# Optimization experiments

Measured on AMD Instinct MI355X. Metric: run time of the kernel, lower is better.

The kernel has to match this reference:

```python
import jax, jax.numpy as jnp
import numpy as np

TEMP_LEN, TARGET_LEN = 16, 22
NT, NA = TEMP_LEN ** 2, TARGET_LEN ** 2  # 256, 484
N = NT + NA  # 740
DIM, HEADS = 512, 8
HD = DIM // HEADS
SCALE = HD ** -0.5
BATCH = 16


def _bias_index(L):
    # Swin-style relative position index for an LxL grid -> [L^2, L^2] ints
    coords = np.stack(np.meshgrid(np.arange(L), np.arange(L), indexing='ij')).reshape(2, -1)
    rel = (coords[:, :, None] - coords[:, None, :]).transpose(1, 2, 0).copy()
    rel[..., 0] += L - 1
    rel[..., 1] += L - 1
    rel[..., 0] *= 2 * L - 1
    return jnp.asarray(rel.sum(-1))


TEMP_IDX = _bias_index(TEMP_LEN)
TARGET_IDX = _bias_index(TARGET_LEN)


def _conv_bn(x, w, g, b, m, v):
    # depthwise 3x3 conv (groups=DIM), then BatchNorm in inference form
    y = jax.lax.conv_general_dilated(x, w, (1, 1), 'SAME', feature_group_count=DIM,
                                     dimension_numbers=('NCHW', 'OIHW', 'NCHW'))
    inv = g * jax.lax.rsqrt(v + 1e-5)
    return y * inv[None, :, None, None] + (b - m * inv)[None, :, None, None]


def _forward(x, wcq, wck, wcv,
             bnq_g, bnq_b, bnq_m, bnq_v,
             bnk_g, bnk_b, bnk_m, bnk_v,
             bnv_g, bnv_b, bnv_m, bnv_v,
             wq, wk, wv, wproj, bproj,
             rpb_target, rpb_temp, t2a_table, a2t_table, t2a_line, a2t_line):
    B = x.shape[0]
    temp = jnp.transpose(x[:, :NT], (0, 2, 1)).reshape(B, DIM, TEMP_LEN, TEMP_LEN)
    target = jnp.transpose(x[:, NT:], (0, 2, 1)).reshape(B, DIM, TARGET_LEN, TARGET_LEN)

    def proj_tokens(w, g, b, m, v):
        ytm = _conv_bn(temp, w, g, b, m, v).reshape(B, DIM, NT).transpose(0, 2, 1)
        yta = _conv_bn(target, w, g, b, m, v).reshape(B, DIM, NA).transpose(0, 2, 1)
        return jnp.concatenate([ytm, yta], axis=1)  # [B, N, DIM]

    q = proj_tokens(wcq, bnq_g, bnq_b, bnq_m, bnq_v)
    k = proj_tokens(wck, bnk_g, bnk_b, bnk_m, bnk_v)
    v = proj_tokens(wcv, bnv_g, bnv_b, bnv_m, bnv_v)

    # linear (no bias), split heads -> [B, H, N, HD]
    def heads(y, w):
        return jnp.einsum('bnc,dc->bnd', y, w).reshape(B, N, HEADS, HD).transpose(0, 2, 1, 3)

    q, k, v = heads(q, wq), heads(k, wk), heads(v, wv)

    # relative position bias, assembled blockwise -> [H, N, N]
    temp_b = rpb_temp[TEMP_IDX.reshape(-1)].reshape(NT, NT, HEADS).transpose(2, 0, 1)
    target_b = rpb_target[TARGET_IDX.reshape(-1)].reshape(NA, NA, HEADS).transpose(2, 0, 1)
    top_right = t2a_table + a2t_line    # [H, NT, NA] (temp queries -> target keys)
    bottom_left = a2t_table + t2a_line  # [H, NA, NT] (target queries -> temp keys)
    bias = jnp.concatenate([
        jnp.concatenate([temp_b, top_right], axis=2),
        jnp.concatenate([bottom_left, target_b], axis=2)], axis=1)

    attn = jnp.einsum('bhnd,bhmd->bhnm', q, k) * SCALE + bias[None]
    attn = jax.nn.softmax(attn, axis=-1)
    out = jnp.einsum('bhnm,bhmd->bhnd', attn, v).transpose(0, 2, 1, 3).reshape(B, N, DIM)
    return jnp.einsum('bnc,dc->bnd', out, wproj) + bproj


def setup_inputs() -> dict:
    key = jax.random.key(0)
    ks = jax.random.split(key, 32)
    d = {}
    d['x'] = jax.random.normal(ks[0], (BATCH, N, DIM), jnp.float32)
    for i, nm in enumerate(['q', 'k', 'v']):
        d['wc' + nm] = jax.random.normal(ks[1 + i], (DIM, 1, 3, 3), jnp.float32) * 0.1
        d['bn%s_g' % nm] = jax.random.uniform(ks[4 + i], (DIM,), jnp.float32, 0.5, 1.5)
        d['bn%s_b' % nm] = jax.random.normal(ks[7 + i], (DIM,), jnp.float32) * 0.1
        d['bn%s_m' % nm] = jax.random.normal(ks[10 + i], (DIM,), jnp.float32) * 0.1
        d['bn%s_v' % nm] = jax.random.uniform(ks[13 + i], (DIM,), jnp.float32, 0.5, 1.5)
        d['w' + nm] = jax.random.normal(ks[16 + i], (DIM, DIM), jnp.float32) * (DIM ** -0.5)
    d['wproj'] = jax.random.normal(ks[19], (DIM, DIM), jnp.float32) * (DIM ** -0.5)
    d['bproj'] = jnp.zeros((DIM,), jnp.float32)
    std = 0.0002
    d['rpb_target'] = jax.random.normal(ks[20], ((2 * TARGET_LEN - 1) ** 2, HEADS), jnp.float32) * std
    d['rpb_temp'] = jax.random.normal(ks[21], ((2 * TEMP_LEN - 1) ** 2, HEADS), jnp.float32) * std
    d['t2a_table'] = jax.random.normal(ks[22], (HEADS, NT, 1), jnp.float32) * std
    d['a2t_table'] = jax.random.normal(ks[23], (HEADS, NA, 1), jnp.float32) * std
    d['t2a_line'] = jax.random.normal(ks[24], (HEADS, 1, NT), jnp.float32) * std
    d['a2t_line'] = jax.random.normal(ks[25], (HEADS, 1, NA), jnp.float32) * std
    return d


def reference(x, wcq, wck, wcv,
              bnq_g, bnq_b, bnq_m, bnq_v,
              bnk_g, bnk_b, bnk_m, bnk_v,
              bnv_g, bnv_b, bnv_m, bnv_v,
              wq, wk, wv, wproj, bproj,
              rpb_target, rpb_temp, t2a_table, a2t_table, t2a_line, a2t_line):
    return _forward(x, wcq, wck, wcv,
                    bnq_g, bnq_b, bnq_m, bnq_v,
                    bnk_g, bnk_b, bnk_m, bnk_v,
                    bnv_g, bnv_b, bnv_m, bnv_v,
                    wq, wk, wv, wproj, bproj,
                    rpb_target, rpb_temp, t2a_table, a2t_table, t2a_line, a2t_line)
```

## Files before the change

### kernel.cpp

```cpp
#include <hip/hip_runtime.h>
#include <hip/hip_bf16.h>
#include <cstdint>
#include <cstddef>

typedef __hip_bfloat16 bf16;
typedef float  f32x4 __attribute__((ext_vector_type(4)));
typedef short  s16x8 __attribute__((ext_vector_type(8)));
typedef short  s16x4 __attribute__((ext_vector_type(4)));

#define NB    16
#define NTOK  740
#define NTMP  256
#define NTGT  484
#define DIM   512
#define NHEAD 8
#define HD    64
#define MROWS (NB*NTOK)
#define WOFF  (DIM*DIM)
#define BSTRIDE 768
#define LOG2E 1.44269504f
#define SC2   (0.125f * LOG2E)

#define EXP2F(x) __builtin_amdgcn_exp2f(x)

static __device__ __forceinline__ short f2bs(float f) {
    bf16 h = __float2bfloat16(f);
    return *reinterpret_cast<short*>(&h);
}
static __device__ __forceinline__ float bs2f(short s) {
    union { unsigned int u; float f; } cv;
    cv.u = ((unsigned int)(unsigned short)s) << 16;
    return cv.f;
}

__global__ __launch_bounds__(256) void convert_w_kernel(
    const float* __restrict__ wq, const float* __restrict__ wk,
    const float* __restrict__ wv, const float* __restrict__ wp,
    bf16* __restrict__ out)
{
    const int t = blockIdx.x * 256 + threadIdx.x;
    const int which = t >> 18;
    const int idx   = t & (WOFF - 1);
    const float* src = (which == 0) ? wq : (which == 1) ? wk : (which == 2) ? wv : wp;
    out[t] = __float2bfloat16(src[idx]);
}

__global__ __launch_bounds__(256) void prep_kernel(
    const float* __restrict__ wcq, const float* __restrict__ wck, const float* __restrict__ wcv,
    const float* __restrict__ qg, const float* __restrict__ qb, const float* __restrict__ qm, const float* __restrict__ qv,
    const float* __restrict__ kg, const float* __restrict__ kb, const float* __restrict__ km, const float* __restrict__ kv,
    const float* __restrict__ vg, const float* __restrict__ vb, const float* __restrict__ vm, const float* __restrict__ vv,
    float* __restrict__ wT, float* __restrict__ ss)
{
    const int t = blockIdx.x * 256 + threadIdx.x;
    if (t < 3 * 9 * 512) {
        const int w = t / (9 * 512);
        const int r = t - w * 9 * 512;
        const int s = r >> 9, c = r & 511;
        const float* src = (w == 0) ? wcq : (w == 1) ? wck : wcv;
        wT[t] = src[c * 9 + s];
    } else if (t < 3 * 9 * 512 + 3 * 512) {
        const int u = t - 3 * 9 * 512;
        const int w = u >> 9, c = u & 511;
        const float* G = (w == 0) ? qg : (w == 1) ? kg : vg;
        const float* V = (w == 0) ? qv : (w == 1) ? kv : vv;
        const float* B = (w == 0) ? qb : (w == 1) ? kb : vb;
        const float* M = (w == 0) ? qm : (w == 1) ? km : vm;
        const float inv = G[c] * rsqrtf(V[c] + 1e-5f);
        ss[w * 1024 + c]       = inv;
        ss[w * 1024 + 512 + c] = B[c] - M[c] * inv;
    }
}

__global__ __launch_bounds__(256) void bias_prep_kernel(
    const float* __restrict__ rpb_temp, const float* __restrict__ rpb_target,
    const float* __restrict__ t2a_tab, const float* __restrict__ a2t_tab,
    const float* __restrict__ t2a_line, const float* __restrict__ a2t_line,
    bf16* __restrict__ biasp)
{
    const int t = blockIdx.x * 256 + threadIdx.x;
    if (t >= NHEAD * NTOK * (BSTRIDE / 4)) return;
    const int kg = t % (BSTRIDE / 4);
    const int hq = t / (BSTRIDE / 4);
    const int qq = hq % NTOK;
    const int h  = hq / NTOK;

    bool tq; int qi, qj; float tab;
    if (qq < NTMP) { tq = true;  qi = qq >> 4; qj = qq & 15; tab = t2a_tab[h * NTMP + qq]; }
    else { tq = false; int qa = qq - NTMP; qi = qa / 22; qj = qa - qi * 22; tab = a2t_tab[h * NTGT + qa]; }

    s16x4 o;
    #pragma unroll
    for (int r = 0; r < 4; ++r) {
        const int key = kg * 4 + r;
        float bias = 0.f;
        if (key < NTOK) {
            if (tq) {
                if (key < NTMP) {
                    const int ki = key >> 4, kj = key & 15;
                    bias = rpb_temp[((qi - ki + 15) * 31 + (qj - kj + 15)) * NHEAD + h];
                } else bias = tab + a2t_line[h * NTGT + key - NTMP];
            } else {
                if (key < NTMP) bias = tab + t2a_line[h * NTMP + key];
                else {
                    const int ka = key - NTMP;
                    const int ki = ka / 22, kj = ka - ki * 22;
                    bias = rpb_target[((qi - ki + 21) * 43 + (qj - kj + 21)) * NHEAD + h];
                }
            }
        }
        o[r] = f2bs(bias * LOG2E);
    }
    *reinterpret_cast<s16x4*>(biasp + ((size_t)h * NTOK + qq) * BSTRIDE + kg * 4) = o;
}

__global__ __launch_bounds__(256) void conv_bn_kernel(
    const float* __restrict__ x,
    const float* __restrict__ wT, const float* __restrict__ ss,
    bf16* __restrict__ qc, bf16* __restrict__ kc, bf16* __restrict__ vc)
{
    const int t   = blockIdx.x * 256 + threadIdx.x;
    const int c0  = (t & 127) * 4;
    const int idx = t >> 7;
    const int b   = idx / NTOK;
    const int n   = idx - b * NTOK;

    int li, lj, L, base;
    if (n < NTMP) { L = 16; li = n >> 4; lj = n & 15; base = 0; }
    else          { int a = n - NTMP; L = 22; li = a / 22; lj = a - li * 22; base = NTMP; }

    const float* xb = x + (size_t)b * NTOK * DIM + c0;

    float4 xs[9];
    #pragma unroll
    for (int di = -1; di <= 1; ++di)
        #pragma unroll
        for (int dj = -1; dj <= 1; ++dj) {
            int ii = li + di, jj = lj + dj;
            float4 xv = make_float4(0.f, 0.f, 0.f, 0.f);
            if ((unsigned)ii < (unsigned)L && (unsigned)jj < (unsigned)L)
                xv = *reinterpret_cast<const float4*>(xb + (size_t)(base + ii * L + jj) * DIM);
            xs[(di + 1) * 3 + (dj + 1)] = xv;
        }

#define DO_CONV(OUT, W)                                                        \
    if (OUT) {                                                                 \
        float4 acc = make_float4(0.f, 0.f, 0.f, 0.f);                          \
        _Pragma("unroll")                                                      \
        for (int s = 0; s < 9; ++s) {                                          \
            const float4 w4 = *reinterpret_cast<const float4*>(wT + (W) * 4608 + s * 512 + c0); \
            acc.x += xs[s].x * w4.x; acc.y += xs[s].y * w4.y;                  \
            acc.z += xs[s].z * w4.z; acc.w += xs[s].w * w4.w;                  \
        }                                                                      \
        const float4 iv = *reinterpret_cast<const float4*>(ss + (W) * 1024 + c0);        \
        const float4 sh = *reinterpret_cast<const float4*>(ss + (W) * 1024 + 512 + c0);  \
        ushort4 o;                                                             \
        o.x = (unsigned short)f2bs(acc.x * iv.x + sh.x);                       \
        o.y = (unsigned short)f2bs(acc.y * iv.y + sh.y);                       \
        o.z = (unsigned short)f2bs(acc.z * iv.z + sh.z);                       \
        o.w = (unsigned short)f2bs(acc.w * iv.w + sh.w);                       \
        *reinterpret_cast<ushort4*>(OUT + (size_t)idx * DIM + c0) = o;         \
    }
    DO_CONV(qc, 0)
    DO_CONV(kc, 1)
    DO_CONV(vc, 2)
#undef DO_CONV
}

__global__ __launch_bounds__(256) void gemm_bt(
    const bf16* __restrict__ Abase,
    const bf16* __restrict__ W0, const bf16* __restrict__ W1, const bf16* __restrict__ W2,
    bf16* __restrict__ Cbase, float* __restrict__ Cf, const float* __restrict__ bias)
{
    __shared__ bf16 lA[128 * 32];
    __shared__ bf16 lB[128 * 32];

    const int tid  = threadIdx.x;
    const int lane = tid & 63;
    const int wid  = tid >> 6;
    const int lq   = lane & 15, lg = lane >> 4;
    const int wr   = wid >> 1,  wc = wid & 1;
    const int z    = blockIdx.z;

    const bf16* A = Abase + (size_t)z * MROWS * DIM;
    const bf16* W = (z == 0) ? W0 : ((z == 1) ? W1 : W2);
    bf16*       C = Cbase ? (Cbase + (size_t)z * MROWS * DIM) : nullptr;

    const int bm = blockIdx.x, bn = blockIdx.y;

    const int srow = wid * 16 + (lane >> 2);
    const int scol = (lane & 3) * 8;
    const int rowA0 = min(bm * 128 + srow,      MROWS - 1);
    const int rowA1 = min(bm * 128 + 64 + srow, MROWS - 1);
    const int rowB0 = bn * 128 + srow;
    const int rowB1 = rowB0 + 64;

    f32x4 acc[4][4];
    #pragma unroll
    for (int m = 0; m < 4; ++m)
        #pragma unroll
        for (int n = 0; n < 4; ++n) acc[m][n] = (f32x4){0.f, 0.f, 0.f, 0.f};

    for (int ks = 0; ks < 16; ++ks) {
        const int k0 = ks * 32 + scol;
        __builtin_amdgcn_global_load_lds(
            (const __attribute__((address_space(1))) void*)(A + (size_t)rowA0 * DIM + k0),
            (__attribute__((address_space(3))) void*)(lA + wid * 512), 16, 0, 0);
        __builtin_amdgcn_global_load_lds(
            (const __attribute__((address_space(1))) void*)(A + (size_t)rowA1 * DIM + k0),
            (__attribute__((address_space(3))) void*)(lA + (wid + 4) * 512), 16, 0, 0);
        __builtin_amdgcn_global_load_lds(
            (const __attribute__((address_space(1))) void*)(W + (size_t)rowB0 * DIM + k0),
            (__attribute__((address_space(3))) void*)(lB + wid * 512), 16, 0, 0);
        __builtin_amdgcn_global_load_lds(
            (const __attribute__((address_space(1))) void*)(W + (size_t)rowB1 * DIM + k0),
            (__attribute__((address_space(3))) void*)(lB + (wid + 4) * 512), 16, 0, 0);
        __syncthreads();

        s16x8 af[4], bf_[4];
        #pragma unroll
        for (int m = 0; m < 4; ++m)
            af[m] = *reinterpret_cast<const s16x8*>(&lA[(wr * 64 + m * 16 + lq) * 32 + lg * 8]);
        #pragma unroll
        for (int n = 0; n < 4; ++n)
            bf_[n] = *reinterpret_cast<const s16x8*>(&lB[(wc * 64 + n * 16 + lq) * 32 + lg * 8]);

        #pragma unroll
        for (int m = 0; m < 4; ++m)
            #pragma unroll
            for (int n = 0; n < 4; ++n)
                acc[m][n] = __builtin_amdgcn_mfma_f32_16x16x32_bf16(af[m], bf_[n], acc[m][n], 0, 0, 0);
        __syncthreads();
    }

    #pragma unroll
    for (int m = 0; m < 4; ++m) {
        const int row = bm * 128 + wr * 64 + m * 16 + lg * 4;
        #pragma unroll
        for (int n = 0; n < 4; ++n) {
            const int col = bn * 128 + wc * 64 + n * 16 + lq;
            const float bv = bias ? bias[col] : 0.f;
            #pragma unroll
            for (int r = 0; r < 4; ++r) {
                const int rr = row + r;
                if (rr < MROWS) {
                    const float val = acc[m][n][r] + bv;
                    if (Cf) Cf[(size_t)rr * DIM + col] = val;
                    else    C [(size_t)rr * DIM + col] = __float2bfloat16(val);
                }
            }
        }
    }
}

__global__ __launch_bounds__(256) void attn_kernel(
    const bf16* __restrict__ q, const bf16* __restrict__ k, const bf16* __restrict__ v,
    const bf16* __restrict__ biasp,
    bf16* __restrict__ out)
{
    __shared__ char  lK[64 * 128];
    __shared__ short lVT[64 * 72];

    const int lane = threadIdx.x & 63;
    const int wid  = threadIdx.x >> 6;
    const int lq   = lane & 15, lg = lane >> 4;
    const int h    = blockIdx.y, b = blockIdx.z;

    const size_t bh = (size_t)b * NTOK * DIM + h * HD;
    const bf16* qp = q + bh;
    const bf16* kp = k + bh;
    const bf16* vp = v + bh;

    const int qrA = blockIdx.x * 128 + wid * 32 + lq;
    const int qrB = qrA + 16;
    const int qA  = min(qrA, NTOK - 1);
    const int qB  = min(qrB, NTOK - 1);

    const s16x8 qf0A = *reinterpret_cast<const s16x8*>(qp + (size_t)qA * DIM + lg * 8);
    const s16x8 qf1A = *reinterpret_cast<const s16x8*>(qp + (size_t)qA * DIM + 32 + lg * 8);
    const s16x8 qf0B = *reinterpret_cast<const s16x8*>(qp + (size_t)qB * DIM + lg * 8);
    const s16x8 qf1B = *reinterpret_cast<const s16x8*>(qp + (size_t)qB * DIM + 32 + lg * 8);

    const bf16* bpA = biasp + ((size_t)h * NTOK + qA) * BSTRIDE;
    const bf16* bpB = biasp + ((size_t)h * NTOK + qB) * BSTRIDE;

    float mA = -1e30f, lsA = 0.f, mB = -1e30f, lsB = 0.f;
    f32x4 oA[4], oB[4];
    #pragma unroll
    for (int d = 0; d < 4; ++d) { oA[d] = (f32x4){0,0,0,0}; oB[d] = (f32x4){0,0,0,0}; }

    const int swz     = (((lane & 7) ^ (lane >> 3)) << 4);
    const int krowoff = lane >> 3;

    for (int t = 0; t < 12; ++t) {
        const int kt0 = t * 64;
        __syncthreads();

        #pragma unroll
        for (int c0 = 0; c0 < 2; ++c0) {
            const int c    = wid + c0 * 4;
            const int krow = min(kt0 + c * 8 + krowoff, NTOK - 1);
            __builtin_amdgcn_global_load_lds(
                (const __attribute__((address_space(1))) void*)((const char*)(kp + (size_t)krow * DIM) + swz),
                (__attribute__((address_space(3))) void*)(lK + c * 1024), 16, 0, 0);
        }
        {
            const int vrow = min(kt0 + lane, NTOK - 1);
            const bf16* vsrc = vp + (size_t)vrow * DIM + wid * 16;
            const s16x8 v0 = *reinterpret_cast<const s16x8*>(vsrc);
            const s16x8 v1 = *reinterpret_cast<const s16x8*>(vsrc + 8);
            #pragma unroll
            for (int i = 0; i < 8; ++i) {
                lVT[(wid * 16 + i)     * 72 + lane] = v0[i];
                lVT[(wid * 16 + 8 + i) * 72 + lane] = v1[i];
            }
        }
        s16x4 bA[4], bB[4];
        #pragma unroll
        for (int s = 0; s < 4; ++s) {
            bA[s] = *reinterpret_cast<const s16x4*>(bpA + kt0 + s * 16 + lg * 4);
            bB[s] = *reinterpret_cast<const s16x4*>(bpB + kt0 + s * 16 + lg * 4);
        }
        __syncthreads();

        f32x4 stA[4], stB[4];
        #pragma unroll
        for (int s = 0; s < 4; ++s) {
            const int row = s * 16 + lq;
            const int cb0 = (lg * 16)      ^ ((row & 7) << 4);
            const int cb1 = (64 + lg * 16) ^ ((row & 7) << 4);
            const s16x8 kf0 = *reinterpret_cast<const s16x8*>(lK + row * 128 + cb0);
            const s16x8 kf1 = *reinterpret_cast<const s16x8*>(lK + row * 128 + cb1);
            f32x4 z0 = {0,0,0,0}, z1 = {0,0,0,0};
            z0 = __builtin_amdgcn_mfma_f32_16x16x32_bf16(kf0, qf0A, z0, 0, 0, 0);
            stA[s] = __builtin_amdgcn_mfma_f32_16x16x32_bf16(kf1, qf1A, z0, 0, 0, 0);
            z1 = __builtin_amdgcn_mfma_f32_16x16x32_bf16(kf0, qf0B, z1, 0, 0, 0);
            stB[s] = __builtin_amdgcn_mfma_f32_16x16x32_bf16(kf1, qf1B, z1, 0, 0, 0);
        }

        s16x4 pbA[4], pbB[4];

#define TILE_SOFTMAX(ST, BV, MR, LS, OO, PB)                                    \
        {                                                                       \
            float tmax = -1e30f;                                                \
            _Pragma("unroll")                                                   \
            for (int s = 0; s < 4; ++s) {                                       \
                _Pragma("unroll")                                               \
                for (int r = 0; r < 4; ++r) {                                   \
                    float sv = ST[s][r] * SC2 + bs2f(BV[s][r]);                 \
                    if (kt0 + s * 16 + lg * 4 + r >= NTOK) sv = -1e30f;         \
                    ST[s][r] = sv;                                              \
                    tmax = fmaxf(tmax, sv);                                     \
                }                                                               \
            }                                                                   \
            tmax = fmaxf(tmax, __shfl_xor(tmax, 16));                           \
            tmax = fmaxf(tmax, __shfl_xor(tmax, 32));                           \
            if (tmax > MR) {                                                    \
                const float al = EXP2F(MR - tmax);                              \
                LS *= al;                                                       \
                _Pragma("unroll")                                               \
                for (int d = 0; d < 4; ++d) {                                   \
                    OO[d][0] *= al; OO[d][1] *= al;                             \
                    OO[d][2] *= al; OO[d][3] *= al;                             \
                }                                                               \
                MR = tmax;                                                      \
            }                                                                   \
            float rs = 0.f;                                                     \
            _Pragma("unroll")                                                   \
            for (int s = 0; s < 4; ++s) {                                       \
                _Pragma("unroll")                                               \
                for (int r = 0; r < 4; ++r) {                                   \
                    const float p = EXP2F(ST[s][r] - MR);                       \
                    rs += p;                                                    \
                    PB[s][r] = f2bs(p);                                         \
                }                                                               \
            }                                                                   \
            rs += __shfl_xor(rs, 16);                                           \
            rs += __shfl_xor(rs, 32);                                           \
            LS += rs;                                                           \
        }
        TILE_SOFTMAX(stA, bA, mA, lsA, oA, pbA)
        TILE_SOFTMAX(stB, bB, mB, lsB, oB, pbB)
#undef TILE_SOFTMAX

        #pragma unroll
        for (int s = 0; s < 4; ++s) {
            #pragma unroll
            for (int db = 0; db < 4; ++db) {
                const s16x4 av = *reinterpret_cast<const s16x4*>(
                    lVT + (db * 16 + lq) * 72 + s * 16 + lg * 4);
                oA[db] = __builtin_amdgcn_mfma_f32_16x16x16bf16_1k(av, pbA[s], oA[db], 0, 0, 0);
                oB[db] = __builtin_amdgcn_mfma_f32_16x16x16bf16_1k(av, pbB[s], oB[db], 0, 0, 0);
            }
        }
    }

#define STORE_FRAG(QR, LS, OO)                                                  \
    if ((QR) < NTOK) {                                                          \
        const float inv = 1.f / (LS);                                           \
        bf16* op = out + ((size_t)b * NTOK + (QR)) * DIM + h * HD;              \
        _Pragma("unroll")                                                       \
        for (int db = 0; db < 4; ++db) {                                        \
            ushort4 sv;                                                         \
            sv.x = (unsigned short)f2bs(OO[db][0] * inv);                       \
            sv.y = (unsigned short)f2bs(OO[db][1] * inv);                       \
            sv.z = (unsigned short)f2bs(OO[db][2] * inv);                       \
            sv.w = (unsigned short)f2bs(OO[db][3] * inv);                       \
            *reinterpret_cast<ushort4*>(op + db * 16 + lg * 4) = sv;            \
        }                                                                       \
    }
    STORE_FRAG(qrA, lsA, oA)
    STORE_FRAG(qrB, lsB, oB)
#undef STORE_FRAG
}

extern "C" void kernel_launch(void* const* d_in, const int* in_sizes, int n_in,
                              void* d_out, int out_size, void* d_ws, size_t ws_size,
                              hipStream_t stream)
{
    const bool sig = (in_sizes[2] == 4608);
    const float *x, *wcq, *wck, *wcv, *wq, *wk, *wv, *wproj, *bproj;
    const float *bnqg, *bnqb, *bnqm, *bnqv, *bnkg, *bnkb, *bnkm, *bnkv, *bnvg, *bnvb, *bnvm, *bnvv;
#define P(i) ((const float*)d_in[i])
    x = P(0);
    if (!sig) {
        wcq = P(1);  bnqg = P(2);  bnqb = P(3);  bnqm = P(4);  bnqv = P(5);  wq = P(6);
        wck = P(7);  bnkg = P(8);  bnkb = P(9);  bnkm = P(10); bnkv = P(11); wk = P(12);
        wcv = P(13); bnvg = P(14); bnvb = P(15); bnvm = P(16); bnvv = P(17); wv = P(18);
    } else {
        wcq = P(1);  wck = P(2);  wcv = P(3);
        bnqg = P(4);  bnqb = P(5);  bnqm = P(6);  bnqv = P(7);
        bnkg = P(8);  bnkb = P(9);  bnkm = P(10); bnkv = P(11);
        bnvg = P(12); bnvb = P(13); bnvm = P(14); bnvv = P(15);
        wq = P(16); wk = P(17); wv = P(18);
    }
    wproj = P(19); bproj = P(20);
    const float* rpbt = P(21);
    const float* rpbm = P(22);
    const float* t2at = P(23);
    const float* a2tt = P(24);
    const float* t2al = P(25);
    const float* a2tl = P(26);
#undef P

    const size_t BUF    = (size_t)MROWS * DIM;
    const size_t WELEMS = (size_t)4 * WOFF;
    const size_t PREPF  = 17408;
    const size_t BIASE  = (size_t)NHEAD * NTOK * BSTRIDE;

    bf16*  wsW   = (bf16*)d_ws;
    float* wsF   = (float*)(wsW + WELEMS);
    float* wT    = wsF;
    float* ssb   = wsF + 3 * 9 * 512;
    bf16*  biasP = (bf16*)(wsF + PREPF);
    bf16*  bufs  = biasP + BIASE;

    convert_w_kernel<<<dim3(WELEMS / 256), 256, 0, stream>>>(wq, wk, wv, wproj, wsW);
    prep_kernel<<<dim3(60), 256, 0, stream>>>(
        wcq, wck, wcv,
        bnqg, bnqb, bnqm, bnqv, bnkg, bnkb, bnkm, bnkv, bnvg, bnvb, bnvm, bnvv,
        wT, ssb);
    bias_prep_kernel<<<dim3((NHEAD * NTOK * (BSTRIDE / 4) + 255) / 256), 256, 0, stream>>>(
        rpbm, rpbt, t2at, a2tt, t2al, a2tl, biasP);

    const bool big = ws_size >= (WELEMS * 2 + PREPF * 4 + BIASE * 2 + 6 * BUF * 2);

    if (big) {
        bf16* qc = bufs + 0 * BUF;
        bf16* kc = bufs + 1 * BUF;
        bf16* vc = bufs + 2 * BUF;
        bf16* qh = bufs + 3 * BUF;
        bf16* ao = qc;

        conv_bn_kernel<<<dim3(MROWS * 128 / 256), 256, 0, stream>>>(x, wT, ssb, qc, kc, vc);

        gemm_bt<<<dim3(93, 4, 3), 256, 0, stream>>>(qc, wsW, wsW + WOFF, wsW + 2 * WOFF,
                                                    qh, nullptr, nullptr);

        attn_kernel<<<dim3(6, NHEAD, NB), 256, 0, stream>>>(
            qh, qh + BUF, qh + 2 * BUF, biasP, ao);

        gemm_bt<<<dim3(93, 4, 1), 256, 0, stream>>>(ao, wsW + 3 * WOFF, nullptr, nullptr,
                                                    nullptr, (float*)d_out, bproj);
    } else {
        bf16* b0 = bufs + 0 * BUF;
        bf16* b1 = bufs + 1 * BUF;
        bf16* b2 = bufs + 2 * BUF;
        bf16* b3 = bufs + 3 * BUF;

        conv_bn_kernel<<<dim3(MROWS * 128 / 256), 256, 0, stream>>>(x, wT, ssb, b0, nullptr, nullptr);
        gemm_bt<<<dim3(93, 4, 1), 256, 0, stream>>>(b0, wsW, nullptr, nullptr, b1, nullptr, nullptr);

        conv_bn_kernel<<<dim3(MROWS * 128 / 256), 256, 0, stream>>>(x, wT, ssb, nullptr, b0, nullptr);
        gemm_bt<<<dim3(93, 4, 1), 256, 0, stream>>>(b0, wsW + WOFF, nullptr, nullptr, b2, nullptr, nullptr);

        conv_bn_kernel<<<dim3(MROWS * 128 / 256), 256, 0, stream>>>(x, wT, ssb, nullptr, nullptr, b0);
        gemm_bt<<<dim3(93, 4, 1), 256, 0, stream>>>(b0, wsW + 2 * WOFF, nullptr, nullptr, b3, nullptr, nullptr);

        attn_kernel<<<dim3(6, NHEAD, NB), 256, 0, stream>>>(
            b1, b2, b3, biasP, b0);

        gemm_bt<<<dim3(93, 4, 1), 256, 0, stream>>>(b0, wsW + 3 * WOFF, nullptr, nullptr,
                                                    nullptr, (float*)d_out, bproj);
    }
}
```

Baseline: 312.7 us.

## Double-buffer LDS tiles in GEMM and attention kernels to overlap loads with MFMA

Both the projection GEMM and the attention kernel now use two LDS buffers. The next K-slice, or the next K/V tile plus its bias, is prefetched while the MFMAs run on the current one, and there is one barrier per iteration instead of two. The attention loop peels its last tile so the out-of-range mask is applied only there. This doubles LDS use and raises register pressure for the prefetched V and bias values, which may lower occupancy.

```diff
diff --git a/kernel.cpp b/kernel.cpp
--- a/kernel.cpp
+++ b/kernel.cpp
@@ -172,8 +172,8 @@
     const bf16* __restrict__ W0, const bf16* __restrict__ W1, const bf16* __restrict__ W2,
     bf16* __restrict__ Cbase, float* __restrict__ Cf, const float* __restrict__ bias)
 {
-    __shared__ bf16 lA[128 * 32];
-    __shared__ bf16 lB[128 * 32];
+    __shared__ bf16 lA[2][128 * 32];
+    __shared__ bf16 lB[2][128 * 32];
 
     const int tid  = threadIdx.x;
     const int lane = tid & 63;
@@ -195,35 +195,42 @@
     const int rowB0 = bn * 128 + srow;
     const int rowB1 = rowB0 + 64;
 
+#define GSTAGE(BUF, KS) do {                                                         \
+    const int k0_ = (KS) * 32 + scol;                                                \
+    __builtin_amdgcn_global_load_lds(                                                \
+        (const __attribute__((address_space(1))) void*)(A + (size_t)rowA0 * DIM + k0_), \
+        (__attribute__((address_space(3))) void*)(lA[BUF] + wid * 512), 16, 0, 0);   \
+    __builtin_amdgcn_global_load_lds(                                                \
+        (const __attribute__((address_space(1))) void*)(A + (size_t)rowA1 * DIM + k0_), \
+        (__attribute__((address_space(3))) void*)(lA[BUF] + (wid + 4) * 512), 16, 0, 0); \
+    __builtin_amdgcn_global_load_lds(                                                \
+        (const __attribute__((address_space(1))) void*)(W + (size_t)rowB0 * DIM + k0_), \
+        (__attribute__((address_space(3))) void*)(lB[BUF] + wid * 512), 16, 0, 0);   \
+    __builtin_amdgcn_global_load_lds(                                                \
+        (const __attribute__((address_space(1))) void*)(W + (size_t)rowB1 * DIM + k0_), \
+        (__attribute__((address_space(3))) void*)(lB[BUF] + (wid + 4) * 512), 16, 0, 0); \
+    } while (0)
+
     f32x4 acc[4][4];
     #pragma unroll
     for (int m = 0; m < 4; ++m)
         #pragma unroll
         for (int n = 0; n < 4; ++n) acc[m][n] = (f32x4){0.f, 0.f, 0.f, 0.f};
 
+    GSTAGE(0, 0);
+    __syncthreads();
+
+    int cur = 0;
     for (int ks = 0; ks < 16; ++ks) {
-        const int k0 = ks * 32 + scol;
-        __builtin_amdgcn_global_load_lds(
-            (const __attribute__((address_space(1))) void*)(A + (size_t)rowA0 * DIM + k0),
-            (__attribute__((address_space(3))) void*)(lA + wid * 512), 16, 0, 0);
-        __builtin_amdgcn_global_load_lds(
-            (const __attribute__((address_space(1))) void*)(A + (size_t)rowA1 * DIM + k0),
-            (__attribute__((address_space(3))) void*)(lA + (wid + 4) * 512), 16, 0, 0);
-        __builtin_amdgcn_global_load_lds(
-            (const __attribute__((address_space(1))) void*)(W + (size_t)rowB0 * DIM + k0),
-            (__attribute__((address_space(3))) void*)(lB + wid * 512), 16, 0, 0);
-        __builtin_amdgcn_global_load_lds(
-            (const __attribute__((address_space(1))) void*)(W + (size_t)rowB1 * DIM + k0),
-            (__attribute__((address_space(3))) void*)(lB + (wid + 4) * 512), 16, 0, 0);
-        __syncthreads();
+        if (ks < 15) GSTAGE(cur ^ 1, ks + 1);
 
         s16x8 af[4], bf_[4];
         #pragma unroll
         for (int m = 0; m < 4; ++m)
-            af[m] = *reinterpret_cast<const s16x8*>(&lA[(wr * 64 + m * 16 + lq) * 32 + lg * 8]);
+            af[m] = *reinterpret_cast<const s16x8*>(&lA[cur][(wr * 64 + m * 16 + lq) * 32 + lg * 8]);
         #pragma unroll
         for (int n = 0; n < 4; ++n)
-            bf_[n] = *reinterpret_cast<const s16x8*>(&lB[(wc * 64 + n * 16 + lq) * 32 + lg * 8]);
+            bf_[n] = *reinterpret_cast<const s16x8*>(&lB[cur][(wc * 64 + n * 16 + lq) * 32 + lg * 8]);
 
         #pragma unroll
         for (int m = 0; m < 4; ++m)
@@ -231,7 +238,9 @@
             for (int n = 0; n < 4; ++n)
                 acc[m][n] = __builtin_amdgcn_mfma_f32_16x16x32_bf16(af[m], bf_[n], acc[m][n], 0, 0, 0);
         __syncthreads();
-    }
+        cur ^= 1;
+    }
+#undef GSTAGE
 
     #pragma unroll
     for (int m = 0; m < 4; ++m) {
@@ -258,8 +267,8 @@
     const bf16* __restrict__ biasp,
     bf16* __restrict__ out)
 {
-    __shared__ char  lK[64 * 128];
-    __shared__ short lVT[64 * 72];
+    __shared__ char  lK[2][64 * 128];
+    __shared__ short lVT[2][64 * 72];
 
     const int lane = threadIdx.x & 63;
     const int wid  = threadIdx.x >> 6;
@@ -292,108 +301,137 @@
     const int swz     = (((lane & 7) ^ (lane >> 3)) << 4);
     const int krowoff = lane >> 3;
 
-    for (int t = 0; t < 12; ++t) {
+#define STAGE_K(BUF, KT0) do {                                                          \
+    _Pragma("unroll")                                                                   \
+    for (int c0 = 0; c0 < 2; ++c0) {                                                    \
+        const int c_    = wid + c0 * 4;                                                 \
+        const int krow_ = min((KT0) + c_ * 8 + krowoff, NTOK - 1);                      \
+        __builtin_amdgcn_global_load_lds(                                               \
+            (const __attribute__((address_space(1))) void*)((const char*)(kp + (size_t)krow_ * DIM) + swz), \
+            (__attribute__((address_space(3))) void*)(lK[BUF] + c_ * 1024), 16, 0, 0);  \
+    } } while (0)
+
+#define VLOAD(KT0, V0, V1) do {                                                         \
+    const int vrow_ = min((KT0) + lane, NTOK - 1);                                      \
+    const bf16* vsrc_ = vp + (size_t)vrow_ * DIM + wid * 16;                            \
+    V0 = *reinterpret_cast<const s16x8*>(vsrc_);                                        \
+    V1 = *reinterpret_cast<const s16x8*>(vsrc_ + 8); } while (0)
+
+#define VWRITE(BUF, V0, V1) do {                                                        \
+    _Pragma("unroll")                                                                   \
+    for (int i = 0; i < 8; ++i) {                                                       \
+        lVT[BUF][(wid * 16 + i)     * 72 + lane] = V0[i];                               \
+        lVT[BUF][(wid * 16 + 8 + i) * 72 + lane] = V1[i];                               \
+    } } while (0)
+
+#define BLOAD(KT0, BA, BB) do {                                                         \
+    _Pragma("unroll")                                                                   \
+    for (int s = 0; s < 4; ++s) {                                                       \
+        BA[s] = *reinterpret_cast<const s16x4*>(bpA + (KT0) + s * 16 + lg * 4);         \
+        BB[s] = *reinterpret_cast<const s16x4*>(bpB + (KT0) + s * 16 + lg * 4);         \
+    } } while (0)
+
+#define TILE_SOFTMAX(ST, BV, MR, LS, OO, PB, KT0, MASK)                                 \
+        {                                                                               \
+            float tmax = -1e30f;                                                        \
+            _Pragma("unroll")                                                           \
+            for (int s = 0; s < 4; ++s) {                                               \
+                _Pragma("unroll")                                                       \
+                for (int r = 0; r < 4; ++r) {                                           \
+                    float sv = ST[s][r] * SC2 + bs2f(BV[s][r]);                         \
+                    if ((MASK) && (KT0) + s * 16 + lg * 4 + r >= NTOK) sv = -1e30f;     \
+                    ST[s][r] = sv;                                                      \
+                    tmax = fmaxf(tmax, sv);                                             \
+                }                                                                       \
+            }                                                                           \
+            tmax = fmaxf(tmax, __shfl_xor(tmax, 16));                                   \
+            tmax = fmaxf(tmax, __shfl_xor(tmax, 32));                                   \
+            if (tmax > MR) {                                                            \
+                const float al = EXP2F(MR - tmax);                                      \
+                LS *= al;                                                               \
+                _Pragma("unroll")                                                       \
+                for (int d = 0; d < 4; ++d) {                                           \
+                    OO[d][0] *= al; OO[d][1] *= al;                                     \
+                    OO[d][2] *= al; OO[d][3] *= al;                                     \
+                }                                                                       \
+                MR = tmax;                                                              \
+            }                                                                           \
+            float rs = 0.f;                                                             \
+            _Pragma("unroll")                                                           \
+            for (int s = 0; s < 4; ++s) {                                               \
+                _Pragma("unroll")                                                       \
+                for (int r = 0; r < 4; ++r) {                                           \
+                    const float p = EXP2F(ST[s][r] - MR);                               \
+                    rs += p;                                                            \
+                    PB[s][r] = f2bs(p);                                                 \
+                }                                                                       \
+            }                                                                           \
+            rs += __shfl_xor(rs, 16);                                                   \
+            rs += __shfl_xor(rs, 32);                                                   \
+            LS += rs;                                                                   \
+        }
+
+#define TILE_COMPUTE(CUR, KT0, BA, BB, MASK) do {                                       \
+        f32x4 stA[4], stB[4];                                                           \
+        _Pragma("unroll")                                                               \
+        for (int s = 0; s < 4; ++s) {                                                   \
+            const int row_ = s * 16 + lq;                                               \
+            const int cb0_ = (lg * 16) ^ ((row_ & 7) << 4);                             \
+            const s16x8 kf0 = *reinterpret_cast<const s16x8*>(lK[CUR] + row_ * 128 + cb0_);        \
+            const s16x8 kf1 = *reinterpret_cast<const s16x8*>(lK[CUR] + row_ * 128 + (cb0_ ^ 64)); \
+            f32x4 z0 = {0,0,0,0}, z1 = {0,0,0,0};                                       \
+            z0 = __builtin_amdgcn_mfma_f32_16x16x32_bf16(kf0, qf0A, z0, 0, 0, 0);       \
+            stA[s] = __builtin_amdgcn_mfma_f32_16x16x32_bf16(kf1, qf1A, z0, 0, 0, 0);   \
+            z1 = __builtin_amdgcn_mfma_f32_16x16x32_bf16(kf0, qf0B, z1, 0, 0, 0);       \
+            stB[s] = __builtin_amdgcn_mfma_f32_16x16x32_bf16(kf1, qf1B, z1, 0, 0, 0);   \
+        }                                                                               \
+        s16x4 pbA[4], pbB[4];                                                           \
+        TILE_SOFTMAX(stA, BA, mA, lsA, oA, pbA, KT0, MASK)                              \
+        TILE_SOFTMAX(stB, BB, mB, lsB, oB, pbB, KT0, MASK)                              \
+        _Pragma("unroll")                                                               \
+        for (int s = 0; s < 4; ++s) {                                                   \
+            _Pragma("unroll")                                                           \
+            for (int db = 0; db < 4; ++db) {                                            \
+                const s16x4 av = *reinterpret_cast<const s16x4*>(                       \
+                    lVT[CUR] + (db * 16 + lq) * 72 + s * 16 + lg * 4);                  \
+                oA[db] = __builtin_amdgcn_mfma_f32_16x16x16bf16_1k(av, pbA[s], oA[db], 0, 0, 0); \
+                oB[db] = __builtin_amdgcn_mfma_f32_16x16x16bf16_1k(av, pbB[s], oB[db], 0, 0, 0); \
+            }                                                                           \
+        } } while (0)
+
+    STAGE_K(0, 0);
+    s16x8 v0, v1;
+    VLOAD(0, v0, v1);
+    s16x4 bA[4], bB[4];
+    BLOAD(0, bA, bB);
+    VWRITE(0, v0, v1);
+    __syncthreads();
+
+    int cur = 0;
+    for (int t = 0; t < 11; ++t) {
         const int kt0 = t * 64;
+        STAGE_K(cur ^ 1, kt0 + 64);
+        s16x8 v0n, v1n;
+        VLOAD(kt0 + 64, v0n, v1n);
+        s16x4 bAn[4], bBn[4];
+        BLOAD(kt0 + 64, bAn, bBn);
+
+        TILE_COMPUTE(cur, kt0, bA, bB, false);
+
+        VWRITE(cur ^ 1, v0n, v1n);
+        #pragma unroll
+        for (int s = 0; s < 4; ++s) { bA[s] = bAn[s]; bB[s] = bBn[s]; }
         __syncthreads();
-
-        #pragma unroll
-        for (int c0 = 0; c0 < 2; ++c0) {
-            const int c    = wid + c0 * 4;
-            const int krow = min(kt0 + c * 8 + krowoff, NTOK - 1);
-            __builtin_amdgcn_global_load_lds(
-                (const __attribute__((address_space(1))) void*)((const char*)(kp + (size_t)krow * DIM) + swz),
-                (__attribute__((address_space(3))) void*)(lK + c * 1024), 16, 0, 0);
-        }
-        {
-            const int vrow = min(kt0 + lane, NTOK - 1);
-            const bf16* vsrc = vp + (size_t)vrow * DIM + wid * 16;
-            const s16x8 v0 = *reinterpret_cast<const s16x8*>(vsrc);
-            const s16x8 v1 = *reinterpret_cast<const s16x8*>(vsrc + 8);
-            #pragma unroll
-            for (int i = 0; i < 8; ++i) {
-                lVT[(wid * 16 + i)     * 72 + lane] = v0[i];
-                lVT[(wid * 16 + 8 + i) * 72 + lane] = v1[i];
-            }
-        }
-        s16x4 bA[4], bB[4];
-        #pragma unroll
-        for (int s = 0; s < 4; ++s) {
-            bA[s] = *reinterpret_cast<const s16x4*>(bpA + kt0 + s * 16 + lg * 4);
-            bB[s] = *reinterpret_cast<const s16x4*>(bpB + kt0 + s * 16 + lg * 4);
-        }
-        __syncthreads();
-
-        f32x4 stA[4], stB[4];
-        #pragma unroll
-        for (int s = 0; s < 4; ++s) {
-            const int row = s * 16 + lq;
-            const int cb0 = (lg * 16)      ^ ((row & 7) << 4);
-            const int cb1 = (64 + lg * 16) ^ ((row & 7) << 4);
-            const s16x8 kf0 = *reinterpret_cast<const s16x8*>(lK + row * 128 + cb0);
-            const s16x8 kf1 = *reinterpret_cast<const s16x8*>(lK + row * 128 + cb1);
-            f32x4 z0 = {0,0,0,0}, z1 = {0,0,0,0};
-            z0 = __builtin_amdgcn_mfma_f32_16x16x32_bf16(kf0, qf0A, z0, 0, 0, 0);
-            stA[s] = __builtin_amdgcn_mfma_f32_16x16x32_bf16(kf1, qf1A, z0, 0, 0, 0);
-            z1 = __builtin_amdgcn_mfma_f32_16x16x32_bf16(kf0, qf0B, z1, 0, 0, 0);
-            stB[s] = __builtin_amdgcn_mfma_f32_16x16x32_bf16(kf1, qf1B, z1, 0, 0, 0);
-        }
-
-        s16x4 pbA[4], pbB[4];
-
-#define TILE_SOFTMAX(ST, BV, MR, LS, OO, PB)                                    \
-        {                                                                       \
-            float tmax = -1e30f;                                                \
-            _Pragma("unroll")                                                   \
-            for (int s = 0; s < 4; ++s) {                                       \
-                _Pragma("unroll")                                               \
-                for (int r = 0; r < 4; ++r) {                                   \
-                    float sv = ST[s][r] * SC2 + bs2f(BV[s][r]);                 \
-                    if (kt0 + s * 16 + lg * 4 + r >= NTOK) sv = -1e30f;         \
-                    ST[s][r] = sv;                                              \
-                    tmax = fmaxf(tmax, sv);                                     \
-                }                                                               \
-            }                                                                   \
-            tmax = fmaxf(tmax, __shfl_xor(tmax, 16));                           \
-            tmax = fmaxf(tmax, __shfl_xor(tmax, 32));                           \
-            if (tmax > MR) {                                                    \
-                const float al = EXP2F(MR - tmax);                              \
-                LS *= al;                                                       \
-                _Pragma("unroll")                                               \
-                for (int d = 0; d < 4; ++d) {                                   \
-                    OO[d][0] *= al; OO[d][1] *= al;                             \
-                    OO[d][2] *= al; OO[d][3] *= al;                             \
-                }                                                               \
-                MR = tmax;                                                      \
-            }                                                                   \
-            float rs = 0.f;                                                     \
-            _Pragma("unroll")                                                   \
-            for (int s = 0; s < 4; ++s) {                                       \
-                _Pragma("unroll")                                               \
-                for (int r = 0; r < 4; ++r) {                                   \
-                    const float p = EXP2F(ST[s][r] - MR);                       \
-                    rs += p;                                                    \
-                    PB[s][r] = f2bs(p);                                         \
-                }                                                               \
-            }                                                                   \
-            rs += __shfl_xor(rs, 16);                                           \
-            rs += __shfl_xor(rs, 32);                                           \
-            LS += rs;                                                           \
-        }
-        TILE_SOFTMAX(stA, bA, mA, lsA, oA, pbA)
-        TILE_SOFTMAX(stB, bB, mB, lsB, oB, pbB)
+        cur ^= 1;
+    }
+    TILE_COMPUTE(cur, 704, bA, bB, true);
+
+#undef TILE_COMPUTE
 #undef TILE_SOFTMAX
-
-        #pragma unroll
-        for (int s = 0; s < 4; ++s) {
-            #pragma unroll
-            for (int db = 0; db < 4; ++db) {
-                const s16x4 av = *reinterpret_cast<const s16x4*>(
-                    lVT + (db * 16 + lq) * 72 + s * 16 + lg * 4);
-                oA[db] = __builtin_amdgcn_mfma_f32_16x16x16bf16_1k(av, pbA[s], oA[db], 0, 0, 0);
-                oB[db] = __builtin_amdgcn_mfma_f32_16x16x16bf16_1k(av, pbB[s], oB[db], 0, 0, 0);
-            }
-        }
-    }
+#undef BLOAD
+#undef VWRITE
+#undef VLOAD
+#undef STAGE_K
 
 #define STORE_FRAG(QR, LS, OO)                                                  \
     if ((QR) < NTOK) {                                                          \
```

Result: no change. 310.6 us (-0.7%).
